# Performance work log

Measured on AMD Instinct MI355X. Metric: run time of the kernel, lower is better.

The kernel has to match this reference:

```python
import jax, jax.numpy as jnp
import numpy as np

B, S, H = 64, 2048, 256
H3 = 3 * H


def setup_inputs() -> dict:
    key = jax.random.key(0)
    ks = jax.random.split(key, 5)
    static = jax.random.normal(ks[0], (B, S, H), dtype=jnp.float32)
    dynamic = jax.random.normal(ks[1], (B, S, H), dtype=jnp.float32)
    decoder_hidden = jax.random.normal(ks[2], (B, H), dtype=jnp.float32)
    # learned params (nn.Parameter in original); scale ~ 1/sqrt(fan_in)
    v = jax.random.normal(ks[3], (1, H3), dtype=jnp.float32) / np.sqrt(H3)
    W = jax.random.normal(ks[4], (H3, H3), dtype=jnp.float32) / np.sqrt(H3)
    return {"static": static, "dynamic": dynamic,
            "decoder_hidden": decoder_hidden, "v": v, "W": W}


def reference(static, dynamic, decoder_hidden, v, W):
    # cat = concat(static[i,j], dynamic[i,j], decoder_hidden[i]) -> [B, S, 3H]
    dec = jnp.broadcast_to(decoder_hidden[:, None, :], static.shape)
    cat = jnp.concatenate([static, dynamic, dec], axis=-1)
    # score[b,s] = v . tanh(W @ cat[b,s])
    hidden = jnp.tanh(jnp.einsum('ok,bsk->bso', W, cat))  # [B, S, 3H]
    scores = jnp.einsum('bso,o->bs', hidden, v[0])        # [B, S]
    return jax.nn.softmax(scores, axis=1)
```

## Files before the change

kernel.cpp:

```cpp
#include <hip/hip_runtime.h>
#include <hip/hip_bf16.h>

#define B_   64
#define S_   2048
#define H_   256
#define H3_  768
#define K_   512
#define MT   64
#define RSTR 1040

typedef __attribute__((ext_vector_type(8))) short  bf16x8;
typedef __attribute__((ext_vector_type(4))) float  f32x4;

__device__ __forceinline__ uint pkbf2(float a, float b) {
    float2 f = make_float2(a, b);
    __hip_bfloat162 h = __float22bfloat162_rn(f);
    return *reinterpret_cast<uint*>(&h);
}

__global__ void pack_w(const float* __restrict__ W, short* __restrict__ wpk) {
    int t = blockIdx.x * 256 + threadIdx.x;
    if (t >= 48 * 16 * 64) return;
    int lane = t & 63;
    int ks   = (t >> 6) & 15;
    int ot   = t >> 10;
    int o  = ot * 16 + (lane & 15);
    int kb = ks * 32 + (lane >> 4) * 8;
    const float* src = W + (size_t)o * H3_ + kb;
    float4 a = ((const float4*)src)[0];
    float4 b = ((const float4*)src)[1];
    uint4 pk;
    pk.x = pkbf2(a.x, a.y);
    pk.y = pkbf2(a.z, a.w);
    pk.z = pkbf2(b.x, b.y);
    pk.w = pkbf2(b.z, b.w);
    *(uint4*)(wpk + (size_t)t * 8) = pk;
}

__global__ void bias_k(const float* __restrict__ W, const float* __restrict__ dec,
                       const float* __restrict__ v, float* __restrict__ bias,
                       float* __restrict__ vsum) {
    if (blockIdx.x == 192) {
        if (threadIdx.x < 64) {
            float s = 0.f;
#pragma unroll
            for (int i = 0; i < 12; ++i) s += v[threadIdx.x + i * 64];
#pragma unroll
            for (int off = 32; off >= 1; off >>= 1) s += __shfl_xor(s, off);
            if (threadIdx.x == 0) vsum[0] = s;
        }
        return;
    }
    int idx = blockIdx.x * 256 + threadIdx.x;
    int b = idx / H3_;
    int o = idx - b * H3_;
    const float4* wr = (const float4*)(W + (size_t)o * H3_ + 2 * H_);
    const float4* dv = (const float4*)(dec + (size_t)b * H_);
    float s = 0.f;
#pragma unroll 8
    for (int k = 0; k < H_ / 4; ++k) {
        float4 a = wr[k], d = dv[k];
        s += a.x * d.x + a.y * d.y + a.z * d.z + a.w * d.w;
    }
    bias[idx] = s;
}

__global__ __launch_bounds__(256, 2)
void score_k(const float* __restrict__ stat, const float* __restrict__ dyn,
             const short* __restrict__ wpk, const float* __restrict__ bias,
             const float* __restrict__ v, const float* __restrict__ vsum,
             float* __restrict__ scores) {
    __shared__ char  aT[MT * RSTR];
    __shared__ float sred[4][MT];

    const int tid  = threadIdx.x;
    const int pos0 = blockIdx.x * MT;
    const int bidx = pos0 >> 11;

    const int wave = tid >> 6;
    const int lane = tid & 63;
    const int lr = lane & 15;
    const int lg = lane >> 4;

    const short* wbase = wpk + (size_t)lane * 8;

    bf16x8 bcur[4];
#pragma unroll
    for (int ni = 0; ni < 4; ++ni)
        bcur[ni] = *(const bf16x8*)(wbase + (size_t)(wave * 4 + ni) * 8192);

#pragma unroll
    for (int bat = 0; bat < 2; ++bat) {
        float4 f0[8], f1[8];
#pragma unroll
        for (int u = 0; u < 8; ++u) {
            int lin = (bat * 8 + u) * 256 + tid;
            int row = lin >> 6;
            int k   = (lin & 63) * 8;
            const float* src = (k < 256)
                ? (stat + (size_t)(pos0 + row) * H_ + k)
                : (dyn  + (size_t)(pos0 + row) * H_ + (k - 256));
            f0[u] = ((const float4*)src)[0];
            f1[u] = ((const float4*)src)[1];
        }
#pragma unroll
        for (int u = 0; u < 8; ++u) {
            int lin = (bat * 8 + u) * 256 + tid;
            int row = lin >> 6;
            int ux  = lin & 63;
            uint4 pk;
            pk.x = pkbf2(f0[u].x, f0[u].y);
            pk.y = pkbf2(f0[u].z, f0[u].w);
            pk.z = pkbf2(f1[u].x, f1[u].y);
            pk.w = pkbf2(f1[u].z, f1[u].w);
            *(uint4*)(aT + row * RSTR + ux * 16) = pk;
        }
    }
    __syncthreads();

    const char* abase = aT + lr * RSTR + lg * 16;

    float sacc[4][4];
#pragma unroll
    for (int mi = 0; mi < 4; ++mi)
#pragma unroll
        for (int j = 0; j < 4; ++j) sacc[mi][j] = 0.f;

    const float C1 = 2.8853900817779268f;

#pragma unroll 1
    for (int pass = 0; pass < 3; ++pass) {
        const int obase = pass * 256 + wave * 64;

        float bv[4], vv2[4];
#pragma unroll
        for (int ni = 0; ni < 4; ++ni) {
            int o = obase + ni * 16 + lr;
            bv[ni]  = bias[bidx * H3_ + o];
            vv2[ni] = -2.0f * v[o];
        }

        f32x4 acc[4][4];
#pragma unroll
        for (int mi = 0; mi < 4; ++mi)
#pragma unroll
            for (int ni = 0; ni < 4; ++ni) {
                f32x4 a = {bv[ni], bv[ni], bv[ni], bv[ni]};
                acc[mi][ni] = a;
            }

        const short* wp0 = wbase + (size_t)(pass * 16 + wave * 4) * 8192;

#pragma unroll 4
        for (int ks = 0; ks < 16; ++ks) {
            const int ksn = (ks + 1) & 15;
            bf16x8 bnx[4];
#pragma unroll
            for (int ni = 0; ni < 4; ++ni)
                bnx[ni] = *(const bf16x8*)(wp0 + ni * 8192 + ksn * 512);
            bf16x8 afr[4];
#pragma unroll
            for (int mi = 0; mi < 4; ++mi)
                afr[mi] = *(const bf16x8*)(abase + mi * 16 * RSTR + ks * 64);
            __builtin_amdgcn_s_setprio(1);
#pragma unroll
            for (int mi = 0; mi < 4; ++mi)
#pragma unroll
                for (int ni = 0; ni < 4; ++ni)
                    acc[mi][ni] = __builtin_amdgcn_mfma_f32_16x16x32_bf16(
                        afr[mi], bcur[ni], acc[mi][ni], 0, 0, 0);
            __builtin_amdgcn_s_setprio(0);
#pragma unroll
            for (int ni = 0; ni < 4; ++ni) bcur[ni] = bnx[ni];
        }

        if (pass < 2) {
            const short* wpn = wbase + (size_t)((pass + 1) * 16 + wave * 4) * 8192;
#pragma unroll
            for (int ni = 0; ni < 4; ++ni)
                bcur[ni] = *(const bf16x8*)(wpn + ni * 8192);
        }

#pragma unroll
        for (int ni = 0; ni < 4; ++ni)
#pragma unroll
            for (int mi = 0; mi < 4; ++mi)
#pragma unroll
                for (int j = 0; j < 4; ++j) {
                    float e = __builtin_amdgcn_exp2f(acc[mi][ni][j] * C1);
                    float r = __builtin_amdgcn_rcpf(e + 1.0f);
                    sacc[mi][j] = fmaf(vv2[ni], r, sacc[mi][j]);
                }
    }

#pragma unroll
    for (int mi = 0; mi < 4; ++mi)
#pragma unroll
        for (int j = 0; j < 4; ++j) {
            float x = sacc[mi][j];
            x += __shfl_xor(x, 1);
            x += __shfl_xor(x, 2);
            x += __shfl_xor(x, 4);
            x += __shfl_xor(x, 8);
            sacc[mi][j] = x;
        }
    if (lr == 0) {
#pragma unroll
        for (int mi = 0; mi < 4; ++mi)
#pragma unroll
            for (int j = 0; j < 4; ++j)
                sred[wave][mi * 16 + lg * 4 + j] = sacc[mi][j];
    }
    __syncthreads();
    if (tid < MT) {
        float s = vsum[0] + sred[0][tid] + sred[1][tid] + sred[2][tid] + sred[3][tid];
        scores[pos0 + tid] = s;
    }
}

__global__ void softmax_k(float* __restrict__ out) {
    const int b = blockIdx.x;
    float* row = out + (size_t)b * S_;
    const int tid  = threadIdx.x;
    const int wave = tid >> 6;
    const int lane = tid & 63;

    float vals[8];
    float m = -1e30f;
#pragma unroll
    for (int i = 0; i < 8; ++i) {
        vals[i] = row[tid + i * 256];
        m = fmaxf(m, vals[i]);
    }
#pragma unroll
    for (int off = 32; off >= 1; off >>= 1) m = fmaxf(m, __shfl_xor(m, off));
    __shared__ float redm[4];
    __shared__ float reds[4];
    if (lane == 0) redm[wave] = m;
    __syncthreads();
    m = fmaxf(fmaxf(redm[0], redm[1]), fmaxf(redm[2], redm[3]));

    float s = 0.f;
#pragma unroll
    for (int i = 0; i < 8; ++i) {
        vals[i] = __expf(vals[i] - m);
        s += vals[i];
    }
#pragma unroll
    for (int off = 32; off >= 1; off >>= 1) s += __shfl_xor(s, off);
    if (lane == 0) reds[wave] = s;
    __syncthreads();
    s = reds[0] + reds[1] + reds[2] + reds[3];
    float inv = 1.0f / s;
#pragma unroll
    for (int i = 0; i < 8; ++i) row[tid + i * 256] = vals[i] * inv;
}

extern "C" void kernel_launch(void* const* d_in, const int* in_sizes, int n_in,
                              void* d_out, int out_size, void* d_ws, size_t ws_size,
                              hipStream_t stream) {
    const float* stat = (const float*)d_in[0];
    const float* dyn  = (const float*)d_in[1];
    const float* dec  = (const float*)d_in[2];
    const float* v    = (const float*)d_in[3];
    const float* W    = (const float*)d_in[4];
    float* out = (float*)d_out;

    short* wpk  = (short*)d_ws;
    float* bias = (float*)((char*)d_ws + (size_t)H3_ * K_ * 2);
    float* vsum = bias + B_ * H3_;

    pack_w <<<(48 * 16 * 64 + 255) / 256, 256, 0, stream>>>(W, wpk);
    bias_k <<<193, 256, 0, stream>>>(W, dec, v, bias, vsum);
    score_k<<<(B_ * S_) / MT, 256, 0, stream>>>(stat, dyn, wpk, bias, v, vsum, out);
    softmax_k<<<B_, 256, 0, stream>>>(out);
}
```

Measured before the change: 136.3 us.

## Split score kernel work across 8 waves with 512-thread blocks

```diff
diff --git a/kernel.cpp b/kernel.cpp
--- a/kernel.cpp
+++ b/kernel.cpp
@@ -65,13 +65,13 @@
     bias[idx] = s;
 }
 
-__global__ __launch_bounds__(256, 2)
+__global__ __launch_bounds__(512, 4)
 void score_k(const float* __restrict__ stat, const float* __restrict__ dyn,
              const short* __restrict__ wpk, const float* __restrict__ bias,
              const float* __restrict__ v, const float* __restrict__ vsum,
              float* __restrict__ scores) {
     __shared__ char  aT[MT * RSTR];
-    __shared__ float sred[4][MT];
+    __shared__ float sred[8][MT];
 
     const int tid  = threadIdx.x;
     const int pos0 = blockIdx.x * MT;
@@ -84,36 +84,34 @@
 
     const short* wbase = wpk + (size_t)lane * 8;
 
-    bf16x8 bcur[4];
-#pragma unroll
-    for (int ni = 0; ni < 4; ++ni)
-        bcur[ni] = *(const bf16x8*)(wbase + (size_t)(wave * 4 + ni) * 8192);
-
-#pragma unroll
-    for (int bat = 0; bat < 2; ++bat) {
-        float4 f0[8], f1[8];
-#pragma unroll
-        for (int u = 0; u < 8; ++u) {
-            int lin = (bat * 8 + u) * 256 + tid;
-            int row = lin >> 6;
-            int k   = (lin & 63) * 8;
-            const float* src = (k < 256)
-                ? (stat + (size_t)(pos0 + row) * H_ + k)
-                : (dyn  + (size_t)(pos0 + row) * H_ + (k - 256));
-            f0[u] = ((const float4*)src)[0];
-            f1[u] = ((const float4*)src)[1];
-        }
-#pragma unroll
-        for (int u = 0; u < 8; ++u) {
-            int lin = (bat * 8 + u) * 256 + tid;
-            int row = lin >> 6;
-            int ux  = lin & 63;
-            uint4 pk;
-            pk.x = pkbf2(f0[u].x, f0[u].y);
-            pk.y = pkbf2(f0[u].z, f0[u].w);
-            pk.z = pkbf2(f1[u].x, f1[u].y);
-            pk.w = pkbf2(f1[u].z, f1[u].w);
-            *(uint4*)(aT + row * RSTR + ux * 16) = pk;
+    bf16x8 bcur[3];
+#pragma unroll
+    for (int ni = 0; ni < 3; ++ni)
+        bcur[ni] = *(const bf16x8*)(wbase + (size_t)(wave * 6 + ni) * 8192);
+
+    {
+        const int kcol = lane * 8;
+        const float* srcbase = (kcol < 256) ? (stat + kcol) : (dyn + (kcol - 256));
+#pragma unroll
+        for (int bat = 0; bat < 2; ++bat) {
+            float4 f0[4], f1[4];
+#pragma unroll
+            for (int u = 0; u < 4; ++u) {
+                int row = (bat * 4 + u) * 8 + wave;
+                const float4* p = (const float4*)(srcbase + (size_t)(pos0 + row) * H_);
+                f0[u] = p[0];
+                f1[u] = p[1];
+            }
+#pragma unroll
+            for (int u = 0; u < 4; ++u) {
+                int row = (bat * 4 + u) * 8 + wave;
+                uint4 pk;
+                pk.x = pkbf2(f0[u].x, f0[u].y);
+                pk.y = pkbf2(f0[u].z, f0[u].w);
+                pk.z = pkbf2(f1[u].x, f1[u].y);
+                pk.w = pkbf2(f1[u].z, f1[u].w);
+                *(uint4*)(aT + row * RSTR + lane * 16) = pk;
+            }
         }
     }
     __syncthreads();
@@ -128,35 +126,35 @@
 
     const float C1 = 2.8853900817779268f;
 
-#pragma unroll 1
-    for (int pass = 0; pass < 3; ++pass) {
-        const int obase = pass * 256 + wave * 64;
-
-        float bv[4], vv2[4];
-#pragma unroll
-        for (int ni = 0; ni < 4; ++ni) {
+#pragma unroll
+    for (int p = 0; p < 2; ++p) {
+        const int obase = wave * 96 + p * 48;
+
+        float bv[3], vv2[3];
+#pragma unroll
+        for (int ni = 0; ni < 3; ++ni) {
             int o = obase + ni * 16 + lr;
             bv[ni]  = bias[bidx * H3_ + o];
             vv2[ni] = -2.0f * v[o];
         }
 
-        f32x4 acc[4][4];
+        f32x4 acc[4][3];
 #pragma unroll
         for (int mi = 0; mi < 4; ++mi)
 #pragma unroll
-            for (int ni = 0; ni < 4; ++ni) {
+            for (int ni = 0; ni < 3; ++ni) {
                 f32x4 a = {bv[ni], bv[ni], bv[ni], bv[ni]};
                 acc[mi][ni] = a;
             }
 
-        const short* wp0 = wbase + (size_t)(pass * 16 + wave * 4) * 8192;
+        const short* wp0 = wbase + (size_t)(wave * 6 + p * 3) * 8192;
 
 #pragma unroll 4
         for (int ks = 0; ks < 16; ++ks) {
             const int ksn = (ks + 1) & 15;
-            bf16x8 bnx[4];
-#pragma unroll
-            for (int ni = 0; ni < 4; ++ni)
+            bf16x8 bnx[3];
+#pragma unroll
+            for (int ni = 0; ni < 3; ++ni)
                 bnx[ni] = *(const bf16x8*)(wp0 + ni * 8192 + ksn * 512);
             bf16x8 afr[4];
 #pragma unroll
@@ -166,23 +164,23 @@
 #pragma unroll
             for (int mi = 0; mi < 4; ++mi)
 #pragma unroll
-                for (int ni = 0; ni < 4; ++ni)
+                for (int ni = 0; ni < 3; ++ni)
                     acc[mi][ni] = __builtin_amdgcn_mfma_f32_16x16x32_bf16(
                         afr[mi], bcur[ni], acc[mi][ni], 0, 0, 0);
             __builtin_amdgcn_s_setprio(0);
 #pragma unroll
-            for (int ni = 0; ni < 4; ++ni) bcur[ni] = bnx[ni];
-        }
-
-        if (pass < 2) {
-            const short* wpn = wbase + (size_t)((pass + 1) * 16 + wave * 4) * 8192;
-#pragma unroll
-            for (int ni = 0; ni < 4; ++ni)
+            for (int ni = 0; ni < 3; ++ni) bcur[ni] = bnx[ni];
+        }
+
+        if (p == 0) {
+            const short* wpn = wbase + (size_t)(wave * 6 + 3) * 8192;
+#pragma unroll
+            for (int ni = 0; ni < 3; ++ni)
                 bcur[ni] = *(const bf16x8*)(wpn + ni * 8192);
         }
 
 #pragma unroll
-        for (int ni = 0; ni < 4; ++ni)
+        for (int ni = 0; ni < 3; ++ni)
 #pragma unroll
             for (int mi = 0; mi < 4; ++mi)
 #pragma unroll
@@ -213,7 +211,9 @@
     }
     __syncthreads();
     if (tid < MT) {
-        float s = vsum[0] + sred[0][tid] + sred[1][tid] + sred[2][tid] + sred[3][tid];
+        float s = vsum[0];
+#pragma unroll
+        for (int w = 0; w < 8; ++w) s += sred[w][tid];
         scores[pos0 + tid] = s;
     }
 }
@@ -272,6 +272,6 @@
 
     pack_w <<<(48 * 16 * 64 + 255) / 256, 256, 0, stream>>>(W, wpk);
     bias_k <<<193, 256, 0, stream>>>(W, dec, v, bias, vsum);
-    score_k<<<(B_ * S_) / MT, 256, 0, stream>>>(stat, dyn, wpk, bias, v, vsum, out);
+    score_k<<<(B_ * S_) / MT, 512, 0, stream>>>(stat, dyn, wpk, bias, v, vsum, out);
     softmax_k<<<B_, 256, 0, stream>>>(out);
 }
```

New measurement: 167.1 us. 1.23x slower.
